# Kernel tuning notes

Measured on AMD Instinct MI355X. Metric: run time of the kernel, lower is better.

The kernel has to match this reference:

```python
import jax, jax.numpy as jnp
import numpy as np

NUM_CLASSES = 2
THRESHOLD = 0.5
NEGPOS_RATIO = 3
VAR0, VAR1 = 0.1, 0.2  # self.variance = [0.1, 0.2]


def point_form(priors):
    # [cx,cy,w,h] -> [xmin,ymin,xmax,ymax]
    return jnp.concatenate([priors[:, :2] - priors[:, 2:] / 2,
                            priors[:, :2] + priors[:, 2:] / 2], axis=1)


def jaccard(a, b):
    # a: [O,4], b: [P,4] point-form -> IoU [O,P]
    tl = jnp.maximum(a[:, None, :2], b[None, :, :2])
    br = jnp.minimum(a[:, None, 2:], b[None, :, 2:])
    wh = jnp.clip(br - tl, 0.0)
    inter = wh[..., 0] * wh[..., 1]
    area_a = ((a[:, 2] - a[:, 0]) * (a[:, 3] - a[:, 1]))[:, None]
    area_b = ((b[:, 2] - b[:, 0]) * (b[:, 3] - b[:, 1]))[None, :]
    return inter / (area_a + area_b - inter)


def encode(matched, priors):
    # matched: [P,4] point-form GT, priors: [P,4] center-size
    g_cxcy = ((matched[:, :2] + matched[:, 2:]) / 2 - priors[:, :2]) / (VAR0 * priors[:, 2:])
    g_wh = jnp.log((matched[:, 2:] - matched[:, :2]) / priors[:, 2:]) / VAR1
    return jnp.concatenate([g_cxcy, g_wh], axis=1)


def match_one(truths, labels, priors):
    # truths: [O,4], labels: [O], priors: [P,4]
    O = truths.shape[0]
    overlaps = jaccard(truths, point_form(priors))          # [O,P]
    best_prior_idx = jnp.argmax(overlaps, axis=1)           # [O] best prior per GT
    best_truth_overlap = jnp.max(overlaps, axis=0)          # [P]
    best_truth_idx = jnp.argmax(overlaps, axis=0)           # [P]
    # ensure each GT keeps its best prior
    best_truth_overlap = best_truth_overlap.at[best_prior_idx].set(2.0)
    best_truth_idx = best_truth_idx.at[best_prior_idx].set(jnp.arange(O))
    matches = truths[best_truth_idx]                        # [P,4]
    conf = labels[best_truth_idx].astype(jnp.int32)         # head label == 1
    conf = jnp.where(best_truth_overlap < THRESHOLD, 0, conf)
    loc = encode(matches, priors)                           # [P,4]
    return loc, conf


def setup_inputs() -> dict:
    key = jax.random.key(0)
    k1, k2, k3, k4, k5, k6 = jax.random.split(key, 6)
    B, P, O = 32, 32768, 32
    loc_data = jax.random.normal(k1, (B, P, 3), jnp.float32) * 0.1
    conf_data = jax.random.normal(k2, (B, P, 2), jnp.float32)
    cxy = jax.random.uniform(k3, (P, 2), jnp.float32, 0.1, 0.9)
    wh = jax.random.uniform(k4, (P, 2), jnp.float32, 0.05, 0.2)
    priors = jnp.concatenate([cxy, wh], axis=1)
    xy1 = jax.random.uniform(k5, (B, O, 2), jnp.float32, 0.0, 0.7)
    twh = jax.random.uniform(k6, (B, O, 2), jnp.float32, 0.05, 0.25)
    targets = jnp.concatenate([xy1, xy1 + twh, jnp.ones((B, O, 1), jnp.float32)], axis=2)
    return {"loc_data": loc_data, "conf_data": conf_data, "priors": priors, "targets": targets}


def reference(loc_data, conf_data, priors, targets):
    B, P, _ = loc_data.shape
    # convert_coord: [cx, cy, gw] -> [cx, cy, gw, gw]
    quard = jnp.stack([loc_data[..., 0], loc_data[..., 1],
                       loc_data[..., 2], loc_data[..., 2]], axis=-1)  # [B,P,4]
    truths = targets[..., :4]
    labels = targets[..., 4]
    loc_t, conf_t = jax.vmap(lambda t, l: match_one(t, l, priors))(truths, labels)
    pos = conf_t > 0                                         # [B,P]
    # localization smooth-L1 over positives (sum reduction)
    d = quard - loc_t
    ad = jnp.abs(d)
    sl1 = jnp.where(ad < 1.0, 0.5 * d * d, ad - 0.5)
    loss_l = jnp.sum(sl1 * pos[..., None].astype(sl1.dtype))
    # per-prior CE for hard-negative mining
    lse = jax.nn.logsumexp(conf_data, axis=-1)               # [B,P]
    picked = jnp.take_along_axis(conf_data, conf_t[..., None], axis=-1)[..., 0]
    ce = lse - picked                                        # [B,P]
    ce_mine = jnp.where(pos, 0.0, ce)
    # double argsort -> rank of each prior by mining loss (descending)
    loss_idx = jnp.argsort(-ce_mine, axis=1)
    idx_rank = jnp.argsort(loss_idx, axis=1)
    num_pos = jnp.sum(pos.astype(jnp.int32), axis=1, keepdims=True)  # [B,1]
    num_neg = jnp.minimum(NEGPOS_RATIO * num_pos, P - 1)
    neg = idx_rank < num_neg
    sel = jnp.logical_or(pos, neg)
    loss_c = jnp.sum(jnp.where(sel, ce, 0.0))
    N = jnp.sum(num_pos).astype(loss_l.dtype)
    return loss_l / N, loss_c / N
```

## Files before the change

### kernel.cpp

```cpp
#include <hip/hip_runtime.h>
#include <math.h>

#define Bn 32
#define Pn 32768
#define On 32
#define TPB 256
#define PPT 4
#define BP  (TPB * PPT)
#define AG 8
#define AC 1024


__device__ __forceinline__ unsigned long long shfl_down_u64(unsigned long long v, int off) {
    unsigned lo = (unsigned)(v & 0xFFFFFFFFull);
    unsigned hi = (unsigned)(v >> 32);
    lo = __shfl_down(lo, off, 64);
    hi = __shfl_down(hi, off, 64);
    return ((unsigned long long)hi << 32) | lo;
}

__global__ __launch_bounds__(256) void matchA(const float4* __restrict__ priors,
                                              const float* __restrict__ targets,
                                              unsigned long long* __restrict__ bpm) {
    int g    = blockIdx.x;
    int base = blockIdx.y * AC;
    int tid  = threadIdx.x;

    __shared__ float4 tb[AG];
    __shared__ float  ta[AG];
    __shared__ unsigned long long sbest[AG];

    if (tid < AG) {
        const float* t = targets + (size_t)(g * AG + tid) * 5;
        float x1 = t[0], y1 = t[1], x2 = t[2], y2 = t[3];
        tb[tid] = make_float4(x1, y1, x2, y2);
        ta[tid] = (x2 - x1) * (y2 - y1);
        sbest[tid] = 0ull;
    }
    __syncthreads();

    float px1[4], py1[4], px2[4], py2[4], ab[4];
#pragma unroll
    for (int j = 0; j < 4; j++) {
        float4 pr = priors[base + tid + 256 * j];
        px1[j] = pr.x - pr.z * 0.5f; py1[j] = pr.y - pr.w * 0.5f;
        px2[j] = pr.x + pr.z * 0.5f; py2[j] = pr.y + pr.w * 0.5f;
        ab[j]  = (px2[j] - px1[j]) * (py2[j] - py1[j]);
    }

#pragma unroll
    for (int o = 0; o < AG; o++) {
        float4 tt = tb[o];
        float  a  = ta[o];
        float bI = 0.f, bU = 1.f;
        int   bj = 0;
#pragma unroll
        for (int j = 0; j < 4; j++) {
            float ix1 = fmaxf(tt.x, px1[j]), iy1 = fmaxf(tt.y, py1[j]);
            float ix2 = fminf(tt.z, px2[j]), iy2 = fminf(tt.w, py2[j]);
            float iw = fmaxf(ix2 - ix1, 0.f), ih = fmaxf(iy2 - iy1, 0.f);
            float I = iw * ih;
            float U = a + ab[j] - I;
            if (I * bU > bI * U) { bI = I; bU = U; bj = j; }
        }
        int p = base + tid + 256 * bj;
        float iou = bI / bU;
        unsigned long long key = ((unsigned long long)__float_as_uint(iou) << 32)
                               | (unsigned)(Pn - 1 - p);
#pragma unroll
        for (int off = 32; off > 0; off >>= 1) {
            unsigned long long other = shfl_down_u64(key, off);
            if (other > key) key = other;
        }
        if ((tid & 63) == 0) atomicMax(&sbest[o], key);
    }
    __syncthreads();
    if (tid < AG) atomicMax(&bpm[g * AG + tid], sbest[tid]);
}

__global__ __launch_bounds__(256) void matchB(const float* __restrict__ loc,
                                              const float2* __restrict__ conf2,
                                              const float4* __restrict__ priors,
                                              const float* __restrict__ targets,
                                              const unsigned long long* __restrict__ bpm,
                                              float* __restrict__ ce_mine,
                                              int* __restrict__ num_pos,
                                              float* __restrict__ loss_l_t,
                                              float* __restrict__ ce_t,
                                              int* __restrict__ np_tot) {
    int b = blockIdx.y;
    int base = blockIdx.x * BP;
    int tid = threadIdx.x;

    float2 cc[PPT];
#pragma unroll
    for (int j = 0; j < PPT; j++) cc[j] = conf2[(size_t)b * Pn + base + tid + 256 * j];

    __shared__ float4 tb[On];
    __shared__ float  ta[On], lb[On];
    __shared__ int    forced[BP];
    __shared__ float  sred[12];

#pragma unroll
    for (int j = 0; j < PPT; j++) forced[tid + 256 * j] = -1;
    int sp = -1;
    if (tid < On) {
        const float* t = targets + ((size_t)b * On + tid) * 5;
        float x1 = t[0], y1 = t[1], x2 = t[2], y2 = t[3];
        tb[tid] = make_float4(x1, y1, x2, y2);
        ta[tid] = (x2 - x1) * (y2 - y1);
        lb[tid] = t[4];
        sp = Pn - 1 - (int)(bpm[b * On + tid] & 0xFFFFFFFFull);
    }
    __syncthreads();
    if (tid < On && sp >= base && sp < base + BP)
        atomicMax(&forced[sp - base], tid);
    __syncthreads();

    float px1[PPT], py1[PPT], px2[PPT], py2[PPT], ab[PPT], pcx[PPT], pcy[PPT], pw[PPT], ph[PPT];
#pragma unroll
    for (int j = 0; j < PPT; j++) {
        float4 pr = priors[base + tid + 256 * j];
        pcx[j] = pr.x; pcy[j] = pr.y; pw[j] = pr.z; ph[j] = pr.w;
        px1[j] = pr.x - pr.z * 0.5f; py1[j] = pr.y - pr.w * 0.5f;
        px2[j] = pr.x + pr.z * 0.5f; py2[j] = pr.y + pr.w * 0.5f;
        ab[j]  = (px2[j] - px1[j]) * (py2[j] - py1[j]);
    }

    float bIc[PPT][2], bUc[PPT][2];
    int   bxc[PPT][2];
#pragma unroll
    for (int j = 0; j < PPT; j++)
#pragma unroll
        for (int h = 0; h < 2; h++) { bIc[j][h] = 0.f; bUc[j][h] = 1.f; bxc[j][h] = h * 16; }

#pragma unroll 2
    for (int o16 = 0; o16 < 16; o16++) {
#pragma unroll
        for (int h = 0; h < 2; h++) {
            int o = h * 16 + o16;
            float4 tt = tb[o];
            float  a  = ta[o];
#pragma unroll
            for (int j = 0; j < PPT; j++) {
                float ix1 = fmaxf(tt.x, px1[j]), iy1 = fmaxf(tt.y, py1[j]);
                float ix2 = fminf(tt.z, px2[j]), iy2 = fminf(tt.w, py2[j]);
                float iw = fmaxf(ix2 - ix1, 0.f), ih = fmaxf(iy2 - iy1, 0.f);
                float I = iw * ih;
                float U = a + ab[j] - I;
                if (I * bUc[j][h] > bIc[j][h] * U) { bIc[j][h] = I; bUc[j][h] = U; bxc[j][h] = o; }
            }
        }
    }
    float bI[PPT], bU[PPT];
    int   bx[PPT];
#pragma unroll
    for (int j = 0; j < PPT; j++) {
        bI[j] = bIc[j][0]; bU[j] = bUc[j][0]; bx[j] = bxc[j][0];
        if (bIc[j][1] * bU[j] > bI[j] * bUc[j][1]) { bI[j] = bIc[j][1]; bU[j] = bUc[j][1]; bx[j] = bxc[j][1]; }
    }

    float ll_s = 0.f, pce_s = 0.f, cnt_s = 0.f;
#pragma unroll
    for (int j = 0; j < PPT; j++) {
        int p = base + tid + 256 * j;
        int fo = forced[tid + 256 * j];
        int bidx = (fo >= 0) ? fo : bx[j];
        int cf;
        if (fo >= 0)                      cf = (int)lb[bidx];
        else if (bI[j] >= 0.5f * bU[j])   cf = (int)lb[bidx];
        else                              cf = 0;
        bool pos = cf > 0;

        if (pos) {
            float4 tt = tb[bidx];
            float g0 = ((tt.x + tt.z) * 0.5f - pcx[j]) / (0.1f * pw[j]);
            float g1 = ((tt.y + tt.w) * 0.5f - pcy[j]) / (0.1f * ph[j]);
            float g2 = __logf((tt.z - tt.x) / pw[j]) * 5.0f;
            float g3 = __logf((tt.w - tt.y) / ph[j]) * 5.0f;
            const float* lp = loc + ((size_t)b * Pn + p) * 3;
            float q0 = lp[0], q1 = lp[1], q2 = lp[2];
            float dd[4] = { q0 - g0, q1 - g1, q2 - g2, q2 - g3 };
#pragma unroll
            for (int i = 0; i < 4; i++) {
                float ad = fabsf(dd[i]);
                ll_s += (ad < 1.f) ? 0.5f * dd[i] * dd[i] : (ad - 0.5f);
            }
            cnt_s += 1.f;
        }

        float m = fmaxf(cc[j].x, cc[j].y);
        float lse = m + __logf(__expf(cc[j].x - m) + __expf(cc[j].y - m));
        float ce = lse - (cf ? cc[j].y : cc[j].x);
        if (pos) { pce_s += ce; ce = 0.f; }
        ce_mine[(size_t)b * Pn + p] = fmaxf(ce, 0.f);
    }

#pragma unroll
    for (int off = 32; off > 0; off >>= 1) {
        ll_s  += __shfl_down(ll_s,  off, 64);
        pce_s += __shfl_down(pce_s, off, 64);
        cnt_s += __shfl_down(cnt_s, off, 64);
    }
    int lane = tid & 63, wv = tid >> 6;
    if (lane == 0) { sred[wv * 3] = ll_s; sred[wv * 3 + 1] = pce_s; sred[wv * 3 + 2] = cnt_s; }
    __syncthreads();
    if (tid == 0) {
        float llr = 0, pcer = 0, cntr = 0;
        for (int w = 0; w < 4; w++) { llr += sred[w*3]; pcer += sred[w*3+1]; cntr += sred[w*3+2]; }
        if (llr != 0.f)  atomicAdd(loss_l_t, llr);
        if (pcer != 0.f) atomicAdd(ce_t, pcer);
        int c = (int)cntr;
        if (c) { atomicAdd(&num_pos[b], c); atomicAdd(np_tot, c); }
    }
}

__global__ __launch_bounds__(1024) void topk(const float* __restrict__ ce_mine,
                                             const int* __restrict__ num_pos,
                                             float* __restrict__ ce_t,
                                             const float* __restrict__ loss_l_t,
                                             const int* __restrict__ np_tot,
                                             unsigned* __restrict__ tick,
                                             float* __restrict__ out) {
    int b = blockIdx.x, tid = threadIdx.x;
    const float4* v4 = (const float4*)(ce_mine + (size_t)b * Pn);
    float4 r[8];
#pragma unroll
    for (int i = 0; i < 8; i++) r[i] = v4[i * 1024 + tid];

    int k = 3 * num_pos[b];
    if (k > Pn - 1) k = Pn - 1;

    __shared__ int hist[4][2048];
    __shared__ int wavetot[16];
    __shared__ int waveabove[16];
    __shared__ unsigned long long wcand[16];
    __shared__ unsigned s_lo;
    __shared__ int s_ab;
    __shared__ float ssum[16];
    __shared__ int   scnt[16];

    int lane = tid & 63, wv = tid >> 6;

    if (k > 0) {
        unsigned LO = 0u;
        int AB = 0;

        const int shifts[3] = {20, 9, 0};
        const int nbs[3]    = {2048, 2048, 512};

#pragma unroll
        for (int rd = 0; rd < 3; rd++) {
            int shift = shifts[rd], nb = nbs[rd];
            int* hf = &hist[0][0];
            for (int i = tid; i < 4 * 2048; i += 1024) hf[i] = 0;
            __syncthreads();
            int* myh = hist[wv >> 2];
#pragma unroll
            for (int i = 0; i < 8; i++) {
                float4 rv = r[i];
                float vals[4] = {rv.x, rv.y, rv.z, rv.w};
#pragma unroll
                for (int q = 0; q < 4; q++) {
                    unsigned u = __float_as_uint(vals[q]);
                    unsigned bin = (u - LO) >> shift;
                    if (bin < (unsigned)nb) atomicAdd(&myh[bin], 1);
                }
            }
            __syncthreads();
            int c0 = hist[0][2*tid] + hist[1][2*tid] + hist[2][2*tid] + hist[3][2*tid];
            int c1 = hist[0][2*tid+1] + hist[1][2*tid+1] + hist[2][2*tid+1] + hist[3][2*tid+1];
            int local = c0 + c1;
            int suf = local;
#pragma unroll
            for (int off = 1; off < 64; off <<= 1) {
                int src = lane + off;
                int o = __shfl(suf, src & 63, 64);
                suf += (src < 64) ? o : 0;
            }
            if (lane == 0) wavetot[wv] = suf;
            __syncthreads();
            if (tid == 0) {
                int acc = AB;
                for (int w = 15; w >= 0; w--) { waveabove[w] = acc; acc += wavetot[w]; }
            }
            __syncthreads();
            int S0 = waveabove[wv] + suf;
            int S1 = S0 - c0;
            int cand = -1; unsigned nab = 0;
            if (S0 >= k) { cand = 2*tid;     nab = (unsigned)(S0 - c0); }
            if (S1 >= k) { cand = 2*tid + 1; nab = (unsigned)(S1 - c1); }
            unsigned long long pk = ((unsigned long long)(unsigned)(cand + 1) << 32) | nab;
#pragma unroll
            for (int off = 32; off > 0; off >>= 1) {
                unsigned long long o = shfl_down_u64(pk, off);
                if (o > pk) pk = o;
            }
            if (lane == 0) wcand[wv] = pk;
            __syncthreads();
            if (tid == 0) {
                unsigned long long best = 0;
                for (int w = 0; w < 16; w++) if (wcand[w] > best) best = wcand[w];
                int ci = (int)(best >> 32) - 1;
                s_lo = LO + ((unsigned)ci << shift);
                s_ab = (int)(best & 0xFFFFFFFFu);
            }
            __syncthreads();
            LO = s_lo; AB = s_ab;
        }
        float tau = __uint_as_float(LO);
        float s = 0.f; int c = 0;
#pragma unroll
        for (int i = 0; i < 8; i++) {
            if (r[i].x > tau) { s += r[i].x; c++; }
            if (r[i].y > tau) { s += r[i].y; c++; }
            if (r[i].z > tau) { s += r[i].z; c++; }
            if (r[i].w > tau) { s += r[i].w; c++; }
        }
#pragma unroll
        for (int off = 32; off > 0; off >>= 1) {
            s += __shfl_down(s, off, 64);
            c += __shfl_down(c, off, 64);
        }
        if (lane == 0) { ssum[wv] = s; scnt[wv] = c; }
        __syncthreads();
        if (tid == 0) {
            float st = 0.f; int ct = 0;
            for (int w = 0; w < 16; w++) { st += ssum[w]; ct += scnt[w]; }
            atomicAdd(ce_t, st + (float)(k - ct) * tau);
        }
    }

    if (tid == 0) {
        __threadfence();
        unsigned done = atomicAdd(tick, 1u);
        if (done == (unsigned)(Bn - 1)) {
            float N  = (float)atomicAdd((int*)np_tot, 0);
            float ll = atomicAdd((float*)loss_l_t, 0.f);
            float ce = atomicAdd(ce_t, 0.f);
            out[0] = ll / N;
            out[1] = ce / N;
        }
    }
}

extern "C" void kernel_launch(void* const* d_in, const int* in_sizes, int n_in,
                              void* d_out, int out_size, void* d_ws, size_t ws_size,
                              hipStream_t stream) {
    const float* loc     = (const float*)d_in[0];
    const float* conf    = (const float*)d_in[1];
    const float* priors  = (const float*)d_in[2];
    const float* targets = (const float*)d_in[3];
    float* out = (float*)d_out;

    char* ws = (char*)d_ws;
    unsigned long long* bpm = (unsigned long long*)ws;
    int*   num_pos  = (int*)(ws + 8192);
    float* loss_l_t = (float*)(ws + 8320);
    float* ce_t     = (float*)(ws + 8324);
    int*   np_tot   = (int*)(ws + 8328);
    unsigned* tick  = (unsigned*)(ws + 8332);
    float* ce_mine  = (float*)(ws + 16384);

    hipMemsetAsync(ws, 0, 16384, stream);

    hipLaunchKernelGGL(matchA, dim3((Bn * On) / AG, Pn / AC), dim3(256), 0, stream,
                       (const float4*)priors, targets, bpm);
    hipLaunchKernelGGL(matchB, dim3(Pn / BP, Bn), dim3(256), 0, stream,
                       loc, (const float2*)conf, (const float4*)priors, targets, bpm,
                       ce_mine, num_pos, loss_l_t, ce_t, np_tot);
    hipLaunchKernelGGL(topk, dim3(Bn), dim3(1024), 0, stream,
                       ce_mine, num_pos, ce_t, loss_l_t, np_tot, tick, out);
}
```

Measured before the change: 157.7 us.

## Fuse matchA into matchB with per-batch spin barrier and parallelize topk scans

Merges the per-GT best-prior kernel into the main match kernel, so the GT×prior IoU is computed once and both argmaxes come from the same loop. Blocks of a batch synchronize through a global counter spin-wait before applying the forced matches. This removes a kernel launch and the duplicate IoU pass. The spin barrier relies on all 32×32 blocks being co-resident, which launch_bounds(256,4) is meant to ensure, and it adds shared-memory atomics per GT. The topk kernel also replaces serial thread-0 scans with wave shuffles and clears only the histogram bins in use.

```diff
diff --git a/kernel.cpp b/kernel.cpp
--- a/kernel.cpp
+++ b/kernel.cpp
@@ -7,8 +7,7 @@
 #define TPB 256
 #define PPT 4
 #define BP  (TPB * PPT)
-#define AG 8
-#define AC 1024
+#define NCHUNK (Pn / BP)
 
 
 __device__ __forceinline__ unsigned long long shfl_down_u64(unsigned long long v, int off) {
@@ -19,75 +18,17 @@
     return ((unsigned long long)hi << 32) | lo;
 }
 
-__global__ __launch_bounds__(256) void matchA(const float4* __restrict__ priors,
-                                              const float* __restrict__ targets,
-                                              unsigned long long* __restrict__ bpm) {
-    int g    = blockIdx.x;
-    int base = blockIdx.y * AC;
-    int tid  = threadIdx.x;
-
-    __shared__ float4 tb[AG];
-    __shared__ float  ta[AG];
-    __shared__ unsigned long long sbest[AG];
-
-    if (tid < AG) {
-        const float* t = targets + (size_t)(g * AG + tid) * 5;
-        float x1 = t[0], y1 = t[1], x2 = t[2], y2 = t[3];
-        tb[tid] = make_float4(x1, y1, x2, y2);
-        ta[tid] = (x2 - x1) * (y2 - y1);
-        sbest[tid] = 0ull;
-    }
-    __syncthreads();
-
-    float px1[4], py1[4], px2[4], py2[4], ab[4];
-#pragma unroll
-    for (int j = 0; j < 4; j++) {
-        float4 pr = priors[base + tid + 256 * j];
-        px1[j] = pr.x - pr.z * 0.5f; py1[j] = pr.y - pr.w * 0.5f;
-        px2[j] = pr.x + pr.z * 0.5f; py2[j] = pr.y + pr.w * 0.5f;
-        ab[j]  = (px2[j] - px1[j]) * (py2[j] - py1[j]);
-    }
-
-#pragma unroll
-    for (int o = 0; o < AG; o++) {
-        float4 tt = tb[o];
-        float  a  = ta[o];
-        float bI = 0.f, bU = 1.f;
-        int   bj = 0;
-#pragma unroll
-        for (int j = 0; j < 4; j++) {
-            float ix1 = fmaxf(tt.x, px1[j]), iy1 = fmaxf(tt.y, py1[j]);
-            float ix2 = fminf(tt.z, px2[j]), iy2 = fminf(tt.w, py2[j]);
-            float iw = fmaxf(ix2 - ix1, 0.f), ih = fmaxf(iy2 - iy1, 0.f);
-            float I = iw * ih;
-            float U = a + ab[j] - I;
-            if (I * bU > bI * U) { bI = I; bU = U; bj = j; }
-        }
-        int p = base + tid + 256 * bj;
-        float iou = bI / bU;
-        unsigned long long key = ((unsigned long long)__float_as_uint(iou) << 32)
-                               | (unsigned)(Pn - 1 - p);
-#pragma unroll
-        for (int off = 32; off > 0; off >>= 1) {
-            unsigned long long other = shfl_down_u64(key, off);
-            if (other > key) key = other;
-        }
-        if ((tid & 63) == 0) atomicMax(&sbest[o], key);
-    }
-    __syncthreads();
-    if (tid < AG) atomicMax(&bpm[g * AG + tid], sbest[tid]);
-}
-
-__global__ __launch_bounds__(256) void matchB(const float* __restrict__ loc,
-                                              const float2* __restrict__ conf2,
-                                              const float4* __restrict__ priors,
-                                              const float* __restrict__ targets,
-                                              const unsigned long long* __restrict__ bpm,
-                                              float* __restrict__ ce_mine,
-                                              int* __restrict__ num_pos,
-                                              float* __restrict__ loss_l_t,
-                                              float* __restrict__ ce_t,
-                                              int* __restrict__ np_tot) {
+__global__ __launch_bounds__(256, 4) void match(const float* __restrict__ loc,
+                                                const float2* __restrict__ conf2,
+                                                const float4* __restrict__ priors,
+                                                const float* __restrict__ targets,
+                                                unsigned long long* __restrict__ bpm,
+                                                unsigned* __restrict__ cnt,
+                                                float* __restrict__ ce_mine,
+                                                int* __restrict__ num_pos,
+                                                float* __restrict__ loss_l_t,
+                                                float* __restrict__ ce_t,
+                                                int* __restrict__ np_tot) {
     int b = blockIdx.y;
     int base = blockIdx.x * BP;
     int tid = threadIdx.x;
@@ -98,23 +39,20 @@
 
     __shared__ float4 tb[On];
     __shared__ float  ta[On], lb[On];
+    __shared__ unsigned long long sbest[On];
     __shared__ int    forced[BP];
     __shared__ float  sred[12];
 
 #pragma unroll
     for (int j = 0; j < PPT; j++) forced[tid + 256 * j] = -1;
-    int sp = -1;
     if (tid < On) {
         const float* t = targets + ((size_t)b * On + tid) * 5;
         float x1 = t[0], y1 = t[1], x2 = t[2], y2 = t[3];
         tb[tid] = make_float4(x1, y1, x2, y2);
         ta[tid] = (x2 - x1) * (y2 - y1);
         lb[tid] = t[4];
-        sp = Pn - 1 - (int)(bpm[b * On + tid] & 0xFFFFFFFFull);
-    }
-    __syncthreads();
-    if (tid < On && sp >= base && sp < base + BP)
-        atomicMax(&forced[sp - base], tid);
+        sbest[tid] = 0ull;
+    }
     __syncthreads();
 
     float px1[PPT], py1[PPT], px2[PPT], py2[PPT], ab[PPT], pcx[PPT], pcy[PPT], pw[PPT], ph[PPT];
@@ -127,38 +65,58 @@
         ab[j]  = (px2[j] - px1[j]) * (py2[j] - py1[j]);
     }
 
-    float bIc[PPT][2], bUc[PPT][2];
-    int   bxc[PPT][2];
-#pragma unroll
-    for (int j = 0; j < PPT; j++)
-#pragma unroll
-        for (int h = 0; h < 2; h++) { bIc[j][h] = 0.f; bUc[j][h] = 1.f; bxc[j][h] = h * 16; }
-
-#pragma unroll 2
-    for (int o16 = 0; o16 < 16; o16++) {
-#pragma unroll
-        for (int h = 0; h < 2; h++) {
-            int o = h * 16 + o16;
-            float4 tt = tb[o];
-            float  a  = ta[o];
-#pragma unroll
-            for (int j = 0; j < PPT; j++) {
-                float ix1 = fmaxf(tt.x, px1[j]), iy1 = fmaxf(tt.y, py1[j]);
-                float ix2 = fminf(tt.z, px2[j]), iy2 = fminf(tt.w, py2[j]);
-                float iw = fmaxf(ix2 - ix1, 0.f), ih = fmaxf(iy2 - iy1, 0.f);
-                float I = iw * ih;
-                float U = a + ab[j] - I;
-                if (I * bUc[j][h] > bIc[j][h] * U) { bIc[j][h] = I; bUc[j][h] = U; bxc[j][h] = o; }
-            }
-        }
-    }
-    float bI[PPT], bU[PPT];
-    int   bx[PPT];
-#pragma unroll
-    for (int j = 0; j < PPT; j++) {
-        bI[j] = bIc[j][0]; bU[j] = bUc[j][0]; bx[j] = bxc[j][0];
-        if (bIc[j][1] * bU[j] > bI[j] * bUc[j][1]) { bI[j] = bIc[j][1]; bU[j] = bUc[j][1]; bx[j] = bxc[j][1]; }
-    }
+    float bI[PPT] = {0.f, 0.f, 0.f, 0.f};
+    float bU[PPT] = {1.f, 1.f, 1.f, 1.f};
+    int   bx[PPT] = {1 << 30, 1 << 30, 1 << 30, 1 << 30};
+
+#pragma unroll 4
+    for (int step = 0; step < On; step++) {
+        int o = (step + (tid >> 3)) & (On - 1);
+        float4 tt = tb[o];
+        float  a  = ta[o];
+        float I[PPT], U[PPT];
+#pragma unroll
+        for (int j = 0; j < PPT; j++) {
+            float ix1 = fmaxf(tt.x, px1[j]), iy1 = fmaxf(tt.y, py1[j]);
+            float ix2 = fminf(tt.z, px2[j]), iy2 = fminf(tt.w, py2[j]);
+            float iw = fmaxf(ix2 - ix1, 0.f), ih = fmaxf(iy2 - iy1, 0.f);
+            I[j] = iw * ih;
+            U[j] = a + ab[j] - I[j];
+            float l = I[j] * bU[j], r = bI[j] * U[j];
+            bool up = (l > r) || ((l == r) && (o < bx[j]));
+            if (up) { bI[j] = I[j]; bU[j] = U[j]; bx[j] = o; }
+        }
+        float sI = I[0], sU = U[0];
+        int   sj = 0;
+#pragma unroll
+        for (int j = 1; j < PPT; j++) {
+            float l = I[j] * sU, r = sI * U[j];
+            if (l > r) { sI = I[j]; sU = U[j]; sj = j; }
+        }
+        int p = base + tid + 256 * sj;
+        float iou = sI / sU;
+        unsigned long long key = ((unsigned long long)__float_as_uint(iou) << 32)
+                               | (unsigned)(Pn - 1 - p);
+        atomicMax(&sbest[o], key);
+    }
+    __syncthreads();
+    if (tid < On) atomicMax(&bpm[b * On + tid], sbest[tid]);
+    __syncthreads();
+
+    if (tid == 0) {
+        atomicAdd(&cnt[b], 1u);
+        while (atomicAdd(&cnt[b], 0u) < (unsigned)NCHUNK) {
+            __builtin_amdgcn_s_sleep(2);
+        }
+    }
+    __syncthreads();
+
+    int sp = -1;
+    if (tid < On)
+        sp = Pn - 1 - (int)(atomicMax(&bpm[b * On + tid], 0ull) & 0xFFFFFFFFull);
+    if (tid < On && sp >= base && sp < base + BP)
+        atomicMax(&forced[sp - base], tid);
+    __syncthreads();
 
     float ll_s = 0.f, pce_s = 0.f, cnt_s = 0.f;
 #pragma unroll
@@ -253,7 +211,9 @@
         for (int rd = 0; rd < 3; rd++) {
             int shift = shifts[rd], nb = nbs[rd];
             int* hf = &hist[0][0];
-            for (int i = tid; i < 4 * 2048; i += 1024) hf[i] = 0;
+            for (int i = tid; i < nb; i += 1024) {
+                hf[i] = 0; hf[2048 + i] = 0; hf[4096 + i] = 0; hf[6144 + i] = 0;
+            }
             __syncthreads();
             int* myh = hist[wv >> 2];
 #pragma unroll
@@ -268,10 +228,14 @@
                 }
             }
             __syncthreads();
-            int c0 = hist[0][2*tid] + hist[1][2*tid] + hist[2][2*tid] + hist[3][2*tid];
-            int c1 = hist[0][2*tid+1] + hist[1][2*tid+1] + hist[2][2*tid+1] + hist[3][2*tid+1];
+            int stride2 = nb >> 1;
+            int c0 = 0, c1 = 0, suf = 0;
+            if (tid < stride2 || nb == 2048) {
+                c0 = hist[0][2*tid] + hist[1][2*tid] + hist[2][2*tid] + hist[3][2*tid];
+                c1 = hist[0][2*tid+1] + hist[1][2*tid+1] + hist[2][2*tid+1] + hist[3][2*tid+1];
+            }
             int local = c0 + c1;
-            int suf = local;
+            suf = local;
 #pragma unroll
             for (int off = 1; off < 64; off <<= 1) {
                 int src = lane + off;
@@ -280,16 +244,21 @@
             }
             if (lane == 0) wavetot[wv] = suf;
             __syncthreads();
-            if (tid == 0) {
-                int acc = AB;
-                for (int w = 15; w >= 0; w--) { waveabove[w] = acc; acc += wavetot[w]; }
+            if (wv == 0) {
+                int t = (lane < 16) ? wavetot[lane] : 0;
+#pragma unroll
+                for (int off = 1; off < 16; off <<= 1) {
+                    int o2 = __shfl(t, (lane + off) & 63, 64);
+                    t += ((lane + off) < 16) ? o2 : 0;
+                }
+                if (lane < 16) waveabove[lane] = AB + t - wavetot[lane];
             }
             __syncthreads();
             int S0 = waveabove[wv] + suf;
             int S1 = S0 - c0;
             int cand = -1; unsigned nab = 0;
-            if (S0 >= k) { cand = 2*tid;     nab = (unsigned)(S0 - c0); }
-            if (S1 >= k) { cand = 2*tid + 1; nab = (unsigned)(S1 - c1); }
+            if ((tid < stride2 || nb == 2048) && S0 >= k) { cand = 2*tid;     nab = (unsigned)(S0 - c0); }
+            if ((tid < stride2 || nb == 2048) && S1 >= k) { cand = 2*tid + 1; nab = (unsigned)(S1 - c1); }
             unsigned long long pk = ((unsigned long long)(unsigned)(cand + 1) << 32) | nab;
 #pragma unroll
             for (int off = 32; off > 0; off >>= 1) {
@@ -298,12 +267,18 @@
             }
             if (lane == 0) wcand[wv] = pk;
             __syncthreads();
-            if (tid == 0) {
-                unsigned long long best = 0;
-                for (int w = 0; w < 16; w++) if (wcand[w] > best) best = wcand[w];
-                int ci = (int)(best >> 32) - 1;
-                s_lo = LO + ((unsigned)ci << shift);
-                s_ab = (int)(best & 0xFFFFFFFFu);
+            if (wv == 0) {
+                unsigned long long pk2 = (lane < 16) ? wcand[lane] : 0ull;
+#pragma unroll
+                for (int off = 1; off < 16; off <<= 1) {
+                    unsigned long long o2 = shfl_down_u64(pk2, off);
+                    if (o2 > pk2) pk2 = o2;
+                }
+                if (lane == 0) {
+                    int ci = (int)(pk2 >> 32) - 1;
+                    s_lo = LO + ((unsigned)ci << shift);
+                    s_ab = (int)(pk2 & 0xFFFFFFFFu);
+                }
             }
             __syncthreads();
             LO = s_lo; AB = s_ab;
@@ -360,15 +335,14 @@
     float* ce_t     = (float*)(ws + 8324);
     int*   np_tot   = (int*)(ws + 8328);
     unsigned* tick  = (unsigned*)(ws + 8332);
+    unsigned* cnt   = (unsigned*)(ws + 8336);
     float* ce_mine  = (float*)(ws + 16384);
 
     hipMemsetAsync(ws, 0, 16384, stream);
 
-    hipLaunchKernelGGL(matchA, dim3((Bn * On) / AG, Pn / AC), dim3(256), 0, stream,
-                       (const float4*)priors, targets, bpm);
-    hipLaunchKernelGGL(matchB, dim3(Pn / BP, Bn), dim3(256), 0, stream,
-                       loc, (const float2*)conf, (const float4*)priors, targets, bpm,
-                       ce_mine, num_pos, loss_l_t, ce_t, np_tot);
+    hipLaunchKernelGGL(match, dim3(NCHUNK, Bn), dim3(256), 0, stream,
+                       loc, (const float2*)conf, (const float4*)priors, targets,
+                       bpm, cnt, ce_mine, num_pos, loss_l_t, ce_t, np_tot);
     hipLaunchKernelGGL(topk, dim3(Bn), dim3(1024), 0, stream,
                        ce_mine, num_pos, ce_t, loss_l_t, np_tot, tick, out);
 }
```

After: 176.8 us. +12.1%, slower.
